# Kernel tuning notes

Measured on AMD Instinct MI355X. Metric: run time of the kernel, lower is better.

Reference implementation:

```python
import jax, jax.numpy as jnp
import numpy as np

H = 4096
D = 104
# segment boundaries for the 10 log_softmax groups
SEG = [0, 13, 26, 39, 48, 52, 65, 78, 91, 100, 104]

def setup_inputs() -> dict:
    key = jax.random.key(0)
    ks = jax.random.split(key, 8)
    s_h = 1.0 / np.sqrt(H)
    s_d = 1.0 / np.sqrt(D)
    return {
        "line": jax.random.normal(ks[0], (D,), jnp.float32),
        "hidden": jax.random.normal(ks[1], (H,), jnp.float32),
        "Uw": jax.random.uniform(ks[2], (H, H), jnp.float32, -s_h, s_h),
        "Ub": jax.random.uniform(ks[3], (H,), jnp.float32, -s_h, s_h),
        "Ww": jax.random.uniform(ks[4], (H, D), jnp.float32, -s_d, s_d),
        "Wb": jax.random.uniform(ks[5], (H,), jnp.float32, -s_d, s_d),
        "Vw": jax.random.uniform(ks[6], (D, H), jnp.float32, -s_h, s_h),
        "Vb": jax.random.uniform(ks[7], (D,), jnp.float32, -s_h, s_h),
    }

def reference(line, hidden, Uw, Ub, Ww, Wb, Vw, Vb):
    # h_t = sigmoid(U(hidden) + W(line))
    h_t = jax.nn.sigmoid(Uw @ hidden + Ub + Ww @ line + Wb)  # [H]
    pred = Vw @ h_t + Vb  # [D]
    # segmented log_softmax over the 10 fixed groups, then concat
    pred_logsoft = jnp.concatenate(
        [jax.nn.log_softmax(pred[a:b]) for a, b in zip(SEG[:-1], SEG[1:])]
    )
    return pred_logsoft, h_t
```

## Files before the change

kernel.cpp:

```cpp
#include <hip/hip_runtime.h>
#include <math.h>

#define H 4096
#define D 104

typedef float f32x4 __attribute__((ext_vector_type(4)));

__global__ void __launch_bounds__(256) k_hidden(
    const float* __restrict__ Uw, const float* __restrict__ hidden,
    const float* __restrict__ Ub, const float* __restrict__ Ww,
    const float* __restrict__ line, const float* __restrict__ Wb,
    float* __restrict__ h_out)
{
    __shared__ f32x4 s_h4[H / 4];

    const int tid  = threadIdx.x;
    const int wave = tid >> 6;
    const int lane = tid & 63;
    const int row  = blockIdx.x * 4 + wave;

    const f32x4* __restrict__ hv = (const f32x4*)hidden;
    #pragma unroll
    for (int i = tid; i < H / 4; i += 256)
        s_h4[i] = hv[i];
    __syncthreads();

    const f32x4* __restrict__ u = (const f32x4*)(Uw + (size_t)row * H);

    float acc0 = 0.f, acc1 = 0.f;
    #pragma unroll 4
    for (int k = 0; k < 16; k += 2) {
        const int j0 = lane + k * 64;
        const int j1 = j0 + 64;
        f32x4 a0 = __builtin_nontemporal_load(&u[j0]);
        f32x4 b0 = s_h4[j0];
        f32x4 a1 = __builtin_nontemporal_load(&u[j1]);
        f32x4 b1 = s_h4[j1];
        acc0 += a0.x * b0.x + a0.y * b0.y + a0.z * b0.z + a0.w * b0.w;
        acc1 += a1.x * b1.x + a1.y * b1.y + a1.z * b1.z + a1.w * b1.w;
    }
    float acc = acc0 + acc1;

    const f32x4* __restrict__ w  = (const f32x4*)(Ww + (size_t)row * D);
    const f32x4* __restrict__ lv = (const f32x4*)line;
    if (lane < D / 4) {
        f32x4 a = __builtin_nontemporal_load(&w[lane]);
        f32x4 b = lv[lane];
        acc += a.x * b.x + a.y * b.y + a.z * b.z + a.w * b.w;
    }

    #pragma unroll
    for (int off = 32; off; off >>= 1)
        acc += __shfl_down(acc, off, 64);

    if (lane == 0) {
        float v = acc + Ub[row] + Wb[row];
        h_out[row] = 1.f / (1.f + expf(-v));
    }
}

__global__ void __launch_bounds__(256) k_pred_rows(
    const float* __restrict__ Vw, const float* __restrict__ h_t,
    const float* __restrict__ Vb, float* __restrict__ pred)
{
    __shared__ float r[4];
    const int d    = blockIdx.x;
    const int tid  = threadIdx.x;
    const int wave = tid >> 6;
    const int lane = tid & 63;

    const f32x4* __restrict__ v  = (const f32x4*)(Vw + (size_t)d * H);
    const f32x4* __restrict__ hv = (const f32x4*)h_t;

    float acc = 0.f;
    #pragma unroll
    for (int j4 = tid; j4 < H / 4; j4 += 256) {
        f32x4 x = __builtin_nontemporal_load(&v[j4]);
        f32x4 y = hv[j4];
        acc += x.x * y.x + x.y * y.y + x.z * y.z + x.w * y.w;
    }
    #pragma unroll
    for (int off = 32; off; off >>= 1)
        acc += __shfl_down(acc, off, 64);
    if (lane == 0) r[wave] = acc;
    __syncthreads();
    if (tid == 0)
        pred[d] = r[0] + r[1] + r[2] + r[3] + Vb[d];
}

__global__ void __launch_bounds__(640) k_logsoftmax(
    const float* __restrict__ pred, float* __restrict__ out)
{
    const int seg_a[11] = {0, 13, 26, 39, 48, 52, 65, 78, 91, 100, 104};
    const int s    = threadIdx.x >> 6;
    const int lane = threadIdx.x & 63;
    const int a    = seg_a[s];
    const int len  = seg_a[s + 1] - a;

    float x = (lane < len) ? pred[a + lane] : -INFINITY;
    float m = x;
    #pragma unroll
    for (int off = 32; off; off >>= 1)
        m = fmaxf(m, __shfl_xor(m, off, 64));
    float e = (lane < len) ? expf(x - m) : 0.f;
    float ssum = e;
    #pragma unroll
    for (int off = 32; off; off >>= 1)
        ssum += __shfl_xor(ssum, off, 64);
    if (lane < len) out[a + lane] = x - m - logf(ssum);
}

extern "C" void kernel_launch(void* const* d_in, const int* in_sizes, int n_in,
                              void* d_out, int out_size, void* d_ws, size_t ws_size,
                              hipStream_t stream) {
    const float* line   = (const float*)d_in[0];
    const float* hidden = (const float*)d_in[1];
    const float* Uw     = (const float*)d_in[2];
    const float* Ub     = (const float*)d_in[3];
    const float* Ww     = (const float*)d_in[4];
    const float* Wb     = (const float*)d_in[5];
    const float* Vw     = (const float*)d_in[6];
    const float* Vb     = (const float*)d_in[7];

    float* out  = (float*)d_out;
    float* h_t  = out + D;
    float* pred = (float*)d_ws;

    k_hidden<<<H / 4, 256, 0, stream>>>(Uw, hidden, Ub, Ww, line, Wb, h_t);
    k_pred_rows<<<D, 256, 0, stream>>>(Vw, h_t, Vb, pred);
    k_logsoftmax<<<1, 640, 0, stream>>>(pred, out);
}
```

Before: 20.86 us.

## Stream Uw rows through double-buffered LDS via direct global-to-LDS loads

Loads of the large Uw matrix in the hidden-state kernel now go straight into shared memory with the direct global-to-LDS load builtin. The row is split into 512-column tiles that are double-buffered, so the next tile is fetched while the current one is reduced against the cached hidden vector. The goal is to keep more memory traffic in flight and cut register pressure on a bandwidth-bound GEMV. The cost is a block-wide barrier per tile and reliance on the compiler's wait-count handling for async LDS writes, which may serialise the pipeline. A small dot4 helper tidies the other dot products.

```diff
diff --git a/kernel.cpp b/kernel.cpp
--- a/kernel.cpp
+++ b/kernel.cpp
@@ -3,16 +3,25 @@
 
 #define H 4096
 #define D 104
+#define TCOLS 512
+#define NTILES (H / TCOLS)
 
 typedef float f32x4 __attribute__((ext_vector_type(4)));
+typedef __attribute__((address_space(3))) unsigned int lds_u32;
+typedef const __attribute__((address_space(1))) unsigned int glb_u32;
 
-__global__ void __launch_bounds__(256) k_hidden(
+__device__ __forceinline__ float dot4(f32x4 a, f32x4 b) {
+    return a.x * b.x + a.y * b.y + a.z * b.z + a.w * b.w;
+}
+
+__global__ void __launch_bounds__(256, 4) k_hidden(
     const float* __restrict__ Uw, const float* __restrict__ hidden,
     const float* __restrict__ Ub, const float* __restrict__ Ww,
     const float* __restrict__ line, const float* __restrict__ Wb,
     float* __restrict__ h_out)
 {
     __shared__ f32x4 s_h4[H / 4];
+    __shared__ float s_u[2][4 * TCOLS];
 
     const int tid  = threadIdx.x;
     const int wave = tid >> 6;
@@ -23,21 +32,37 @@
     #pragma unroll
     for (int i = tid; i < H / 4; i += 256)
         s_h4[i] = hv[i];
+
+    const float* __restrict__ grow = Uw + (size_t)row * H;
+
+    #define STAGE(t, buf)                                                     \
+        do {                                                                  \
+            const float* g0 = grow + (t) * TCOLS + 4 * lane;                  \
+            __builtin_amdgcn_global_load_lds(                                 \
+                (glb_u32*)g0,                                                 \
+                (lds_u32*)&s_u[buf][wave * TCOLS + 4 * lane], 16, 0, 0);      \
+            const float* g1 = g0 + 256;                                       \
+            __builtin_amdgcn_global_load_lds(                                 \
+                (glb_u32*)g1,                                                 \
+                (lds_u32*)&s_u[buf][wave * TCOLS + 256 + 4 * lane], 16, 0, 0);\
+        } while (0)
+
+    STAGE(0, 0);
     __syncthreads();
 
-    const f32x4* __restrict__ u = (const f32x4*)(Uw + (size_t)row * H);
+    float acc0 = 0.f, acc1 = 0.f;
+    #pragma unroll
+    for (int t = 0; t < NTILES; ++t) {
+        if (t + 1 < NTILES)
+            STAGE(t + 1, (t + 1) & 1);
 
-    float acc0 = 0.f, acc1 = 0.f;
-    #pragma unroll 4
-    for (int k = 0; k < 16; k += 2) {
-        const int j0 = lane + k * 64;
-        const int j1 = j0 + 64;
-        f32x4 a0 = __builtin_nontemporal_load(&u[j0]);
-        f32x4 b0 = s_h4[j0];
-        f32x4 a1 = __builtin_nontemporal_load(&u[j1]);
-        f32x4 b1 = s_h4[j1];
-        acc0 += a0.x * b0.x + a0.y * b0.y + a0.z * b0.z + a0.w * b0.w;
-        acc1 += a1.x * b1.x + a1.y * b1.y + a1.z * b1.z + a1.w * b1.w;
+        const int c4 = t * (TCOLS / 4);
+        f32x4 u0 = *(const f32x4*)&s_u[t & 1][wave * TCOLS + 4 * lane];
+        f32x4 u1 = *(const f32x4*)&s_u[t & 1][wave * TCOLS + 256 + 4 * lane];
+        acc0 += dot4(u0, s_h4[c4 + lane]);
+        acc1 += dot4(u1, s_h4[c4 + 64 + lane]);
+
+        __syncthreads();
     }
     float acc = acc0 + acc1;
 
@@ -45,8 +70,7 @@
     const f32x4* __restrict__ lv = (const f32x4*)line;
     if (lane < D / 4) {
         f32x4 a = __builtin_nontemporal_load(&w[lane]);
-        f32x4 b = lv[lane];
-        acc += a.x * b.x + a.y * b.y + a.z * b.z + a.w * b.w;
+        acc += dot4(a, lv[lane]);
     }
 
     #pragma unroll
@@ -77,7 +101,7 @@
     for (int j4 = tid; j4 < H / 4; j4 += 256) {
         f32x4 x = __builtin_nontemporal_load(&v[j4]);
         f32x4 y = hv[j4];
-        acc += x.x * y.x + x.y * y.y + x.z * y.z + x.w * y.w;
+        acc += dot4(x, y);
     }
     #pragma unroll
     for (int off = 32; off; off >>= 1)
```

Measured after the change: 25.75 us. 1.23x slower.

## Fuse segmented log-softmax into pred kernel via per-segment atomic counters

Applied to the files above, without the earlier changes.

Removes the separate single-block log-softmax launch. Each pred block writes its value to a padded workspace slot, waits for the store, then atomically increments a per-segment counter. The last block in a segment computes that segment's log-softmax. Counters are reset inside the hidden kernel. This saves one kernel launch and its gap, in exchange for atomics and a relaxed-ordering scheme whose memory visibility depends on s_waitcnt rather than proper fences.

```diff
diff --git a/kernel.cpp b/kernel.cpp
--- a/kernel.cpp
+++ b/kernel.cpp
@@ -3,14 +3,19 @@
 
 #define H 4096
 #define D 104
+#define CSTRIDE 32
 
 typedef float f32x4 __attribute__((ext_vector_type(4)));
+
+__device__ __forceinline__ float dot4(f32x4 a, f32x4 b) {
+    return a.x * b.x + a.y * b.y + a.z * b.z + a.w * b.w;
+}
 
 __global__ void __launch_bounds__(256) k_hidden(
     const float* __restrict__ Uw, const float* __restrict__ hidden,
     const float* __restrict__ Ub, const float* __restrict__ Ww,
     const float* __restrict__ line, const float* __restrict__ Wb,
-    float* __restrict__ h_out)
+    float* __restrict__ h_out, unsigned* __restrict__ segcnt)
 {
     __shared__ f32x4 s_h4[H / 4];
 
@@ -18,6 +23,10 @@
     const int wave = tid >> 6;
     const int lane = tid & 63;
     const int row  = blockIdx.x * 4 + wave;
+
+    if (blockIdx.x == 0 && tid < 10)
+        __hip_atomic_store(&segcnt[tid * CSTRIDE], 0u,
+                           __ATOMIC_RELAXED, __HIP_MEMORY_SCOPE_AGENT);
 
     const f32x4* __restrict__ hv = (const f32x4*)hidden;
     #pragma unroll
@@ -36,8 +45,8 @@
         f32x4 b0 = s_h4[j0];
         f32x4 a1 = __builtin_nontemporal_load(&u[j1]);
         f32x4 b1 = s_h4[j1];
-        acc0 += a0.x * b0.x + a0.y * b0.y + a0.z * b0.z + a0.w * b0.w;
-        acc1 += a1.x * b1.x + a1.y * b1.y + a1.z * b1.z + a1.w * b1.w;
+        acc0 += dot4(a0, b0);
+        acc1 += dot4(a1, b1);
     }
     float acc = acc0 + acc1;
 
@@ -45,8 +54,7 @@
     const f32x4* __restrict__ lv = (const f32x4*)line;
     if (lane < D / 4) {
         f32x4 a = __builtin_nontemporal_load(&w[lane]);
-        f32x4 b = lv[lane];
-        acc += a.x * b.x + a.y * b.y + a.z * b.z + a.w * b.w;
+        acc += dot4(a, lv[lane]);
     }
 
     #pragma unroll
@@ -59,17 +67,19 @@
     }
 }
 
-__global__ void __launch_bounds__(256) k_pred_rows(
+__global__ void __launch_bounds__(256) k_pred(
     const float* __restrict__ Vw, const float* __restrict__ h_t,
-    const float* __restrict__ Vb, float* __restrict__ pred)
+    const float* __restrict__ Vb, float* __restrict__ out,
+    unsigned* __restrict__ segcnt, float* __restrict__ pred)
 {
     __shared__ float r[4];
-    const int d    = blockIdx.x;
+    __shared__ int s_last;
+    const int bid  = blockIdx.x;
     const int tid  = threadIdx.x;
     const int wave = tid >> 6;
     const int lane = tid & 63;
 
-    const f32x4* __restrict__ v  = (const f32x4*)(Vw + (size_t)d * H);
+    const f32x4* __restrict__ v  = (const f32x4*)(Vw + (size_t)bid * H);
     const f32x4* __restrict__ hv = (const f32x4*)h_t;
 
     float acc = 0.f;
@@ -77,37 +87,50 @@
     for (int j4 = tid; j4 < H / 4; j4 += 256) {
         f32x4 x = __builtin_nontemporal_load(&v[j4]);
         f32x4 y = hv[j4];
-        acc += x.x * y.x + x.y * y.y + x.z * y.z + x.w * y.w;
+        acc += dot4(x, y);
     }
     #pragma unroll
     for (int off = 32; off; off >>= 1)
         acc += __shfl_down(acc, off, 64);
     if (lane == 0) r[wave] = acc;
     __syncthreads();
-    if (tid == 0)
-        pred[d] = r[0] + r[1] + r[2] + r[3] + Vb[d];
-}
 
-__global__ void __launch_bounds__(640) k_logsoftmax(
-    const float* __restrict__ pred, float* __restrict__ out)
-{
-    const int seg_a[11] = {0, 13, 26, 39, 48, 52, 65, 78, 91, 100, 104};
-    const int s    = threadIdx.x >> 6;
-    const int lane = threadIdx.x & 63;
-    const int a    = seg_a[s];
-    const int len  = seg_a[s + 1] - a;
+    const int SEG[11] = {0, 13, 26, 39, 48, 52, 65, 78, 91, 100, 104};
+    int sidx = 0;
+    #pragma unroll
+    for (int i = 1; i < 10; ++i)
+        if (bid >= SEG[i]) sidx = i;
+    const int a   = SEG[sidx];
+    const int len = SEG[sidx + 1] - a;
 
-    float x = (lane < len) ? pred[a + lane] : -INFINITY;
-    float m = x;
-    #pragma unroll
-    for (int off = 32; off; off >>= 1)
-        m = fmaxf(m, __shfl_xor(m, off, 64));
-    float e = (lane < len) ? expf(x - m) : 0.f;
-    float ssum = e;
-    #pragma unroll
-    for (int off = 32; off; off >>= 1)
-        ssum += __shfl_xor(ssum, off, 64);
-    if (lane < len) out[a + lane] = x - m - logf(ssum);
+    if (tid == 0) {
+        float pr = r[0] + r[1] + r[2] + r[3] + Vb[bid];
+        __hip_atomic_store(&pred[bid * CSTRIDE], pr,
+                           __ATOMIC_RELAXED, __HIP_MEMORY_SCOPE_AGENT);
+        asm volatile("s_waitcnt vmcnt(0)" ::: "memory");
+        unsigned old = __hip_atomic_fetch_add(&segcnt[sidx * CSTRIDE], 1u,
+                                              __ATOMIC_RELAXED,
+                                              __HIP_MEMORY_SCOPE_AGENT);
+        s_last = (old == (unsigned)(len - 1));
+    }
+    __syncthreads();
+
+    if (s_last && wave == 0) {
+        float x = -INFINITY;
+        if (lane < len)
+            x = __hip_atomic_load(&pred[(a + lane) * CSTRIDE],
+                                  __ATOMIC_RELAXED, __HIP_MEMORY_SCOPE_AGENT);
+        float m = x;
+        #pragma unroll
+        for (int off = 32; off; off >>= 1)
+            m = fmaxf(m, __shfl_xor(m, off, 64));
+        float e = (lane < len) ? expf(x - m) : 0.f;
+        float ssum = e;
+        #pragma unroll
+        for (int off = 32; off; off >>= 1)
+            ssum += __shfl_xor(ssum, off, 64);
+        if (lane < len) out[a + lane] = x - m - logf(ssum);
+    }
 }
 
 extern "C" void kernel_launch(void* const* d_in, const int* in_sizes, int n_in,
@@ -122,11 +145,12 @@
     const float* Vw     = (const float*)d_in[6];
     const float* Vb     = (const float*)d_in[7];
 
-    float* out  = (float*)d_out;
-    float* h_t  = out + D;
-    float* pred = (float*)d_ws;
+    float* out = (float*)d_out;
+    float* h_t = out + D;
 
-    k_hidden<<<H / 4, 256, 0, stream>>>(Uw, hidden, Ub, Ww, line, Wb, h_t);
-    k_pred_rows<<<D, 256, 0, stream>>>(Vw, h_t, Vb, pred);
-    k_logsoftmax<<<1, 640, 0, stream>>>(pred, out);
+    unsigned* segcnt = (unsigned*)d_ws;
+    float*    pred   = (float*)d_ws + 1024;
+
+    k_hidden<<<H / 4, 256, 0, stream>>>(Uw, hidden, Ub, Ww, line, Wb, h_t, segcnt);
+    k_pred<<<D, 256, 0, stream>>>(Vw, h_t, Vb, out, segcnt, pred);
 }
```

Measured after the change: 20.60 us. Within noise of the previous version (-1.2%).
